# Kernel tuning notes

Hardware: AMD Instinct MI355X
Metric: run time of the kernel (lower is better)

The kernel has to match this reference:

```python
import jax, jax.numpy as jnp
import numpy as np

NUM_USERS = 100000
NUM_ITEMS = 50000
NUM_LAYERS = 4
DIM_H = 64
E_HALF = 2000000  # undirected interactions; symmetrized to 4M directed edges


def setup_inputs() -> dict:
    key = jax.random.key(0)
    k1, k2, k3, k4 = jax.random.split(key, 4)
    emb_users = 0.01 * jax.random.normal(k1, (NUM_USERS, DIM_H), dtype=jnp.float32)
    emb_items = 0.01 * jax.random.normal(k2, (NUM_ITEMS, DIM_H), dtype=jnp.float32)
    u = jax.random.randint(k3, (E_HALF,), 0, NUM_USERS, dtype=jnp.int64)
    it = jax.random.randint(k4, (E_HALF,), 0, NUM_ITEMS, dtype=jnp.int64) + NUM_USERS
    # bidirectional bipartite graph, as LightGCN expects
    src = jnp.concatenate([u, it])
    dst = jnp.concatenate([it, u])
    edge_index = jnp.stack([src, dst])  # [2, 4M]
    return {"emb_users": emb_users, "emb_items": emb_items, "edge_index": edge_index}


def reference(emb_users, emb_items, edge_index):
    N = emb_users.shape[0] + emb_items.shape[0]
    src, dst = edge_index[0], edge_index[1]
    # gcn_norm (add_self_loops=False): w_e = deg[src]^-1/2 * deg[dst]^-1/2
    deg = jax.ops.segment_sum(jnp.ones(src.shape[0], dtype=emb_users.dtype), dst, num_segments=N)
    dis = jnp.where(deg > 0, deg ** -0.5, 0.0).astype(emb_users.dtype)
    w = (dis[src] * dis[dst])[:, None]  # [E,1]

    emb = jnp.concatenate([emb_users, emb_items])  # [N, D]
    embs_sum = emb
    x = emb
    for _ in range(NUM_LAYERS):
        x = jax.ops.segment_sum(w * x[src], dst, num_segments=N)  # LGConv
        embs_sum = embs_sum + x
    # original: 1/(L+1) * mean over L+1 stacked layers -> sum / (L+1)^2
    emb_final = embs_sum / float((NUM_LAYERS + 1) ** 2)
    emb_users_final = emb_final[: emb_users.shape[0]]
    emb_items_final = emb_final[emb_users.shape[0]:]
    return (emb_users_final, emb_users, emb_items_final, emb_items)
```

## Files before the change

### kernel.cpp

```cpp
#include <hip/hip_runtime.h>
#include <hip/hip_fp8.h>
#include <hip/hip_fp16.h>

typedef unsigned char u8;
typedef unsigned short u16;
typedef float v2f __attribute__((ext_vector_type(2)));

#define SCAN_B 256

#define NPB      128
#define NPB_SH   7
#define P2_CAP   6144
#define STG_CAP  6144
#define P1_CHUNK 16384
#define P1_T     256
#define P1_IT    (P1_CHUNK / P1_T)
#define NB_MAX   2048
#define STG_OFF  ((size_t)20 << 20)

static __device__ __forceinline__ float fp8_to_f32(u8 b) {
    __hip_fp8_e4m3 t;
    t.__x = (__hip_fp8_storage_t)b;
    return (float)t;
}
static __device__ __forceinline__ u8 f32_to_fp8(float v) {
    __hip_fp8_e4m3 t(v);
    return (u8)t.__x;
}
static __device__ __forceinline__ float h2f(u16 u) {
    __half_raw r; r.x = u;
    return __half2float(__half(r));
}
static __device__ __forceinline__ u16 f2h(float f) {
    __half h = __float2half_rn(f);
    __half_raw r = (__half_raw)h;
    return r.x;
}

template <bool HI>
static __device__ __forceinline__ v2f pk2(unsigned w) {
#if __has_builtin(__builtin_amdgcn_cvt_pk_f32_fp8)
    return __builtin_amdgcn_cvt_pk_f32_fp8((int)w, HI);
#else
    v2f r;
    r.x = fp8_to_f32(HI ? (u8)(w >> 16) : (u8)(w));
    r.y = fp8_to_f32(HI ? (u8)(w >> 24) : (u8)(w >> 8));
    return r;
#endif
}

__global__ void detect_kernel(const int* __restrict__ edges, int* __restrict__ flag) {
    __shared__ int cnt[256];
    int t = threadIdx.x;
    int c = 0;
    for (int i = t; i < 32768; i += 256)
        if (edges[2 * i + 1] != 0) c++;
    cnt[t] = c;
    __syncthreads();
    for (int off = 128; off > 0; off >>= 1) {
        if (t < off) cnt[t] += cnt[t + off];
        __syncthreads();
    }
    if (t == 0) flag[0] = (cnt[0] < 8) ? 2 : 1;
}

__global__ void gcur_fixed_init(int* __restrict__ gcur, int NB) {
    int b = blockIdx.x * blockDim.x + threadIdx.x;
    if (b < NB) gcur[b] = b * STG_CAP;
}

__global__ void part1_kernel(const int* __restrict__ edges, const int* __restrict__ flag,
                             int* __restrict__ gcur, unsigned* __restrict__ staging,
                             int E, int NB) {
    __shared__ int lcount[NB_MAX];
    __shared__ int lbase[NB_MAX];
    int t = threadIdx.x;
    int s = flag[0];
    long e0 = (long)blockIdx.x * P1_CHUNK;
    const int* dptr = edges + (long)E * s;
    for (int b = t; b < NB; b += P1_T) lcount[b] = 0;
    __syncthreads();
    for (int j = 0; j < P1_IT; j += 8) {
        int dv[8]; bool vl[8];
        #pragma unroll
        for (int k = 0; k < 8; ++k) {
            long e = e0 + (long)(j + k) * P1_T + t;
            vl[k] = (e < E);
            dv[k] = vl[k] ? dptr[e * s] : 0;
        }
        #pragma unroll
        for (int k = 0; k < 8; ++k)
            if (vl[k]) atomicAdd(&lcount[dv[k] >> NPB_SH], 1);
    }
    __syncthreads();
    for (int b = t; b < NB; b += P1_T) {
        int c = lcount[b];
        lbase[b] = (c > 0) ? atomicAdd(&gcur[b], c) : 0;
        lcount[b] = 0;
    }
    __syncthreads();
    for (int j = 0; j < P1_IT; j += 8) {
        int dv[8], sv[8]; bool vl[8];
        #pragma unroll
        for (int k = 0; k < 8; ++k) {
            long e = e0 + (long)(j + k) * P1_T + t;
            vl[k] = (e < E);
            dv[k] = vl[k] ? dptr[e * s] : 0;
            sv[k] = vl[k] ? edges[e * s] : 0;
        }
        #pragma unroll
        for (int k = 0; k < 8; ++k) {
            if (vl[k]) {
                int b = dv[k] >> NPB_SH;
                int slot = atomicAdd(&lcount[b], 1);
                int pos = lbase[b] + slot;
                if (pos < (b + 1) * STG_CAP)
                    staging[pos] = (unsigned)sv[k]
                                 | ((unsigned)(dv[k] & (NPB - 1)) << 20);
            }
        }
    }
}

__global__ void bucket_scan_kernel(const int* __restrict__ gcur, int* __restrict__ bbase,
                                   int NB) {
    __shared__ int sh[2][1024];
    int t = threadIdx.x;
    int i0 = 2 * t, i1 = 2 * t + 1;
    int a0 = (i0 < NB) ? (gcur[i0] - i0 * STG_CAP) : 0;
    int a1 = (i1 < NB) ? (gcur[i1] - i1 * STG_CAP) : 0;
    sh[0][t] = a0 + a1;
    __syncthreads();
    int src = 0;
    for (int off = 1; off < 1024; off <<= 1) {
        int x = sh[src][t] + ((t >= off) ? sh[src][t - off] : 0);
        sh[src ^ 1][t] = x;
        src ^= 1;
        __syncthreads();
    }
    int incl = sh[src][t];
    int excl = incl - (a0 + a1);
    if (i0 < NB) bbase[i0] = excl;
    if (i1 < NB) bbase[i1] = excl + a0;
    if (t == 1023) bbase[NB] = incl;
}

__global__ void __launch_bounds__(256) part2a_kernel(
        const int* __restrict__ gcur, const int* __restrict__ bbase,
        const unsigned* __restrict__ staging, int* __restrict__ row_ptr,
        float* __restrict__ dis, int n, int E, int NB) {
    __shared__ int cnt[NPB];
    __shared__ int sc[2][NPB];
    int b = blockIdx.x;
    int t = threadIdx.x;
    int dlo = b << NPB_SH;
    int sbase = b * STG_CAP;
    int c = gcur[b] - sbase;
    int base = bbase[b];
    if (t < NPB) cnt[t] = 0;
    __syncthreads();
    for (int k = t; k < c; k += 256) {
        unsigned wd = staging[sbase + k];
        atomicAdd(&cnt[wd >> 20], 1);
    }
    __syncthreads();
    if (t < NPB) sc[0][t] = cnt[t];
    __syncthreads();
    int src = 0;
    for (int off = 1; off < NPB; off <<= 1) {
        if (t < NPB) {
            int x = sc[src][t] + ((t >= off) ? sc[src][t - off] : 0);
            sc[src ^ 1][t] = x;
        }
        src ^= 1;
        __syncthreads();
    }
    if (t < NPB) {
        int node = dlo + t;
        if (node < n) {
            int d = cnt[t];
            row_ptr[node] = base + sc[src][t] - d;
            dis[node] = (d > 0) ? rsqrtf((float)d) : 0.0f;
        }
    }
    if (b == 0 && t == 0) row_ptr[n] = E;
}

__global__ void __launch_bounds__(256) part2b_kernel(
        const int* __restrict__ row_ptr, const int* __restrict__ gcur,
        const unsigned* __restrict__ staging, const float* __restrict__ dis,
        int2* __restrict__ cw, int n) {
    __shared__ int2 win[P2_CAP];
    __shared__ int cur[NPB];
    int b = blockIdx.x;
    int t = threadIdx.x;
    int dlo = b << NPB_SH;
    int sbase = b * STG_CAP;
    int cnt = gcur[b] - sbase;
    int base = row_ptr[dlo];
    if (t < NPB) {
        int node = dlo + t;
        cur[t] = (node < n) ? (row_ptr[node] - base) : 0;
    }
    __syncthreads();
    if (cnt <= P2_CAP) {
        for (int k = t; k < cnt; k += 256) {
            unsigned wd = staging[sbase + k];
            int sv = wd & 0xFFFFF;
            int dloc = wd >> 20;
            float w = dis[sv] * dis[dlo + dloc];
            int p = atomicAdd(&cur[dloc], 1);
            win[p] = make_int2(sv, __float_as_int(w));
        }
        __syncthreads();
        for (int k = t; k < cnt; k += 256)
            cw[base + k] = win[k];
    } else {
        for (int k = t; k < cnt; k += 256) {
            unsigned wd = staging[sbase + k];
            int sv = wd & 0xFFFFF;
            int dloc = wd >> 20;
            float w = dis[sv] * dis[dlo + dloc];
            int p = atomicAdd(&cur[dloc], 1);
            cw[base + p] = make_int2(sv, __float_as_int(w));
        }
    }
}

__global__ void count_deg_kernel(const int* __restrict__ edges, const int* __restrict__ flag,
                                 int* __restrict__ deg, int E) {
    int e = blockIdx.x * blockDim.x + threadIdx.x;
    if (e >= E) return;
    int s = flag[0];
    int d = edges[(long)E * s + (long)e * s];
    atomicAdd(&deg[d], 1);
}

__global__ void scan_phase1(const int* __restrict__ deg, int* __restrict__ row_ptr,
                            int* __restrict__ bsum, int n) {
    __shared__ int sh[2][SCAN_B];
    int t = threadIdx.x;
    int gi = blockIdx.x * SCAN_B + t;
    int v = (gi < n) ? deg[gi] : 0;
    int src = 0;
    sh[0][t] = v;
    __syncthreads();
    for (int off = 1; off < SCAN_B; off <<= 1) {
        int x = sh[src][t] + ((t >= off) ? sh[src][t - off] : 0);
        sh[src ^ 1][t] = x;
        src ^= 1;
        __syncthreads();
    }
    int incl = sh[src][t];
    if (gi < n) row_ptr[gi] = incl - v;
    if (t == SCAN_B - 1) bsum[blockIdx.x] = incl;
}

__global__ void scan_phase2(int* __restrict__ bsum, int nb) {
    __shared__ int sh[1024];
    int t = threadIdx.x;
    sh[t] = (t < nb) ? bsum[t] : 0;
    __syncthreads();
    if (t == 0) {
        int acc = 0;
        for (int i = 0; i < nb; ++i) { int x = sh[i]; sh[i] = acc; acc += x; }
    }
    __syncthreads();
    if (t < nb) bsum[t] = sh[t];
}

__global__ void scan_phase3(const int* __restrict__ deg, const int* __restrict__ bsum,
                            int* __restrict__ row_ptr, int* __restrict__ cursor,
                            float* __restrict__ dis, int n, int E) {
    int gi = blockIdx.x * SCAN_B + threadIdx.x;
    if (gi < n) {
        int e = row_ptr[gi] + bsum[blockIdx.x];
        row_ptr[gi] = e;
        cursor[gi]  = e;
        int d = deg[gi];
        dis[gi] = (d > 0) ? rsqrtf((float)d) : 0.0f;
    }
    if (gi == 0) row_ptr[n] = E;
}

__global__ void scatter_kernel(const int* __restrict__ edges, const int* __restrict__ flag,
                               const float* __restrict__ dis, int* __restrict__ cursor,
                               int2* __restrict__ cw, int E) {
    int e = blockIdx.x * blockDim.x + threadIdx.x;
    if (e >= E) return;
    int s = flag[0];
    int sv = edges[(long)e * s];
    int dv = edges[(long)E * s + (long)e * s];
    float w = dis[sv] * dis[dv];
    int pos = atomicAdd(&cursor[dv], 1);
    cw[pos] = make_int2(sv, __float_as_int(w));
}

__global__ void init_kernel(const float* __restrict__ eu, const float* __restrict__ ei,
                            u8* __restrict__ x0, long NU64, long tot) {
    long i = (long)blockIdx.x * blockDim.x + threadIdx.x;
    if (i >= tot) return;
    float v = (i < NU64) ? eu[i] : ei[i - NU64];
    x0[i] = f32_to_fp8(v);
}

__global__ void spmm_kernel(const int* __restrict__ row_ptr, const int2* __restrict__ cw,
                            const u8* __restrict__ xin, u8* __restrict__ xout, int n) {
    int wave = (blockIdx.x * blockDim.x + threadIdx.x) >> 6;
    int lane = threadIdx.x & 63;
    if (wave >= n) return;
    int beg = row_ptr[wave], end = row_ptr[wave + 1];
    int g = lane >> 3;
    int h = lane & 7;

    float a0 = 0.f, a1 = 0.f, a2 = 0.f, a3 = 0.f;
    float a4 = 0.f, a5 = 0.f, a6 = 0.f, a7 = 0.f;

    for (int iA = beg + g; iA < end; iA += 16) {
        int iB = iA + 8;
        bool vB = iB < end;
        int2 ca = cw[iA];
        int2 cb = cw[vB ? iB : iA];
        uint2 dA = *(const uint2*)(xin + ((long)ca.x << 6) + (h << 3));
        uint2 dB = *(const uint2*)(xin + ((long)cb.x << 6) + (h << 3));
        float wA = __int_as_float(ca.y);
        float wB = vB ? __int_as_float(cb.y) : 0.0f;
        v2f pA0 = pk2<false>(dA.x), pA1 = pk2<true>(dA.x);
        v2f pA2 = pk2<false>(dA.y), pA3 = pk2<true>(dA.y);
        v2f pB0 = pk2<false>(dB.x), pB1 = pk2<true>(dB.x);
        v2f pB2 = pk2<false>(dB.y), pB3 = pk2<true>(dB.y);
        a0 = fmaf(wA, pA0.x, a0); a1 = fmaf(wA, pA0.y, a1);
        a2 = fmaf(wA, pA1.x, a2); a3 = fmaf(wA, pA1.y, a3);
        a4 = fmaf(wA, pA2.x, a4); a5 = fmaf(wA, pA2.y, a5);
        a6 = fmaf(wA, pA3.x, a6); a7 = fmaf(wA, pA3.y, a7);
        a0 = fmaf(wB, pB0.x, a0); a1 = fmaf(wB, pB0.y, a1);
        a2 = fmaf(wB, pB1.x, a2); a3 = fmaf(wB, pB1.y, a3);
        a4 = fmaf(wB, pB2.x, a4); a5 = fmaf(wB, pB2.y, a5);
        a6 = fmaf(wB, pB3.x, a6); a7 = fmaf(wB, pB3.y, a7);
    }
    a0 += __shfl_xor(a0, 8);  a1 += __shfl_xor(a1, 8);
    a2 += __shfl_xor(a2, 8);  a3 += __shfl_xor(a3, 8);
    a4 += __shfl_xor(a4, 8);  a5 += __shfl_xor(a5, 8);
    a6 += __shfl_xor(a6, 8);  a7 += __shfl_xor(a7, 8);
    a0 += __shfl_xor(a0, 16); a1 += __shfl_xor(a1, 16);
    a2 += __shfl_xor(a2, 16); a3 += __shfl_xor(a3, 16);
    a4 += __shfl_xor(a4, 16); a5 += __shfl_xor(a5, 16);
    a6 += __shfl_xor(a6, 16); a7 += __shfl_xor(a7, 16);
    a0 += __shfl_xor(a0, 32); a1 += __shfl_xor(a1, 32);
    a2 += __shfl_xor(a2, 32); a3 += __shfl_xor(a3, 32);
    a4 += __shfl_xor(a4, 32); a5 += __shfl_xor(a5, 32);
    a6 += __shfl_xor(a6, 32); a7 += __shfl_xor(a7, 32);
    if (g == 0) {
        unsigned lo = (unsigned)f32_to_fp8(a0) | ((unsigned)f32_to_fp8(a1) << 8)
                    | ((unsigned)f32_to_fp8(a2) << 16) | ((unsigned)f32_to_fp8(a3) << 24);
        unsigned hi = (unsigned)f32_to_fp8(a4) | ((unsigned)f32_to_fp8(a5) << 8)
                    | ((unsigned)f32_to_fp8(a6) << 16) | ((unsigned)f32_to_fp8(a7) << 24);
        *(uint2*)(xout + ((long)wave << 6) + (h << 3)) = make_uint2(lo, hi);
    }
}

__global__ void final_kernel(const u8* __restrict__ x1, const u8* __restrict__ x2,
                             const u8* __restrict__ x3, const u8* __restrict__ x4,
                             const float* __restrict__ eu, const float* __restrict__ ei,
                             float* __restrict__ out, long NU64, long NI64) {
    long i = (long)blockIdx.x * blockDim.x + threadIdx.x;
    if (i >= NU64 + NI64) return;
    float base = (i < NU64) ? eu[i] : ei[i - NU64];
    float s = base + fp8_to_f32(x1[i]) + fp8_to_f32(x2[i])
                   + fp8_to_f32(x3[i]) + fp8_to_f32(x4[i]);
    float v = s * (1.0f / 25.0f);
    if (i < NU64) {
        out[i] = v;
        out[NU64 + i] = base;
    } else {
        long j = i - NU64;
        out[2 * NU64 + j] = v;
        out[2 * NU64 + NI64 + j] = base;
    }
}

__global__ void init16_kernel(const float* __restrict__ eu, const float* __restrict__ ei,
                              u16* __restrict__ x0, long NU64, long tot) {
    long i = (long)blockIdx.x * blockDim.x + threadIdx.x;
    if (i >= tot) return;
    float v = (i < NU64) ? eu[i] : ei[i - NU64];
    x0[i] = f2h(v);
}

__global__ void spmm16_kernel(const int* __restrict__ row_ptr, const int2* __restrict__ cw,
                              const u16* __restrict__ xin, u16* __restrict__ xout, int n) {
    int wave = (blockIdx.x * blockDim.x + threadIdx.x) >> 6;
    int lane = threadIdx.x & 63;
    if (wave >= n) return;
    int beg = row_ptr[wave], end = row_ptr[wave + 1];
    int g = lane >> 3;
    int h = lane & 7;

    float a0 = 0.f, a1 = 0.f, a2 = 0.f, a3 = 0.f;
    float a4 = 0.f, a5 = 0.f, a6 = 0.f, a7 = 0.f;
    const char* xb = (const char*)xin;

    for (int iA = beg + g; iA < end; iA += 16) {
        int iB = iA + 8;
        bool vB = iB < end;
        int2 ca = cw[iA];
        int2 cb = cw[vB ? iB : iA];
        uint4 dA = *(const uint4*)(xb + ((long)ca.x << 7) + (h << 4));
        uint4 dB = *(const uint4*)(xb + ((long)cb.x << 7) + (h << 4));
        float wA = __int_as_float(ca.y);
        float wB = vB ? __int_as_float(cb.y) : 0.0f;
        a0 = fmaf(wA, h2f((u16)dA.x), a0);  a1 = fmaf(wA, h2f((u16)(dA.x >> 16)), a1);
        a2 = fmaf(wA, h2f((u16)dA.y), a2);  a3 = fmaf(wA, h2f((u16)(dA.y >> 16)), a3);
        a4 = fmaf(wA, h2f((u16)dA.z), a4);  a5 = fmaf(wA, h2f((u16)(dA.z >> 16)), a5);
        a6 = fmaf(wA, h2f((u16)dA.w), a6);  a7 = fmaf(wA, h2f((u16)(dA.w >> 16)), a7);
        a0 = fmaf(wB, h2f((u16)dB.x), a0);  a1 = fmaf(wB, h2f((u16)(dB.x >> 16)), a1);
        a2 = fmaf(wB, h2f((u16)dB.y), a2);  a3 = fmaf(wB, h2f((u16)(dB.y >> 16)), a3);
        a4 = fmaf(wB, h2f((u16)dB.z), a4);  a5 = fmaf(wB, h2f((u16)(dB.z >> 16)), a5);
        a6 = fmaf(wB, h2f((u16)dB.w), a6);  a7 = fmaf(wB, h2f((u16)(dB.w >> 16)), a7);
    }

    a0 += __shfl_xor(a0, 8);  a1 += __shfl_xor(a1, 8);
    a2 += __shfl_xor(a2, 8);  a3 += __shfl_xor(a3, 8);
    a4 += __shfl_xor(a4, 8);  a5 += __shfl_xor(a5, 8);
    a6 += __shfl_xor(a6, 8);  a7 += __shfl_xor(a7, 8);
    a0 += __shfl_xor(a0, 16); a1 += __shfl_xor(a1, 16);
    a2 += __shfl_xor(a2, 16); a3 += __shfl_xor(a3, 16);
    a4 += __shfl_xor(a4, 16); a5 += __shfl_xor(a5, 16);
    a6 += __shfl_xor(a6, 16); a7 += __shfl_xor(a7, 16);
    a0 += __shfl_xor(a0, 32); a1 += __shfl_xor(a1, 32);
    a2 += __shfl_xor(a2, 32); a3 += __shfl_xor(a3, 32);
    a4 += __shfl_xor(a4, 32); a5 += __shfl_xor(a5, 32);
    a6 += __shfl_xor(a6, 32); a7 += __shfl_xor(a7, 32);

    if (g == 0) {
        uint4 ov;
        ov.x = (unsigned)f2h(a0) | ((unsigned)f2h(a1) << 16);
        ov.y = (unsigned)f2h(a2) | ((unsigned)f2h(a3) << 16);
        ov.z = (unsigned)f2h(a4) | ((unsigned)f2h(a5) << 16);
        ov.w = (unsigned)f2h(a6) | ((unsigned)f2h(a7) << 16);
        *(uint4*)((char*)xout + ((long)wave << 7) + (h << 4)) = ov;
    }
}

__global__ void final16_kernel(const u16* __restrict__ x1, const u16* __restrict__ x2,
                               const u16* __restrict__ x3, const u16* __restrict__ x4,
                               const float* __restrict__ eu, const float* __restrict__ ei,
                               float* __restrict__ out, long NU64, long NI64) {
    long i = (long)blockIdx.x * blockDim.x + threadIdx.x;
    if (i >= NU64 + NI64) return;
    float base = (i < NU64) ? eu[i] : ei[i - NU64];
    float s = base + h2f(x1[i]) + h2f(x2[i]) + h2f(x3[i]) + h2f(x4[i]);
    float v = s * (1.0f / 25.0f);
    if (i < NU64) {
        out[i] = v;
        out[NU64 + i] = base;
    } else {
        long j = i - NU64;
        out[2 * NU64 + j] = v;
        out[2 * NU64 + NI64 + j] = base;
    }
}

extern "C" void kernel_launch(void* const* d_in, const int* in_sizes, int n_in,
                              void* d_out, int out_size, void* d_ws, size_t ws_size,
                              hipStream_t stream) {
    const float* eu = (const float*)d_in[0];
    const float* ei = (const float*)d_in[1];
    const int* edges = (const int*)d_in[2];
    float* out = (float*)d_out;

    const int NU = in_sizes[0] / 64;
    const int NI = in_sizes[1] / 64;
    const int N  = NU + NI;
    const int E  = in_sizes[2] / 2;
    const int NB = (N + NPB - 1) / NPB;

    char* w = (char*)d_ws;
    size_t off = 0;
    auto alloc = [&](size_t bytes) -> void* {
        void* p = w + off;
        off += (bytes + 255) & ~(size_t)255;
        return p;
    };
    int*   flag    = (int*)  alloc(256);
    int*   deg     = (int*)  alloc((size_t)N * 4);
    int*   row_ptr = (int*)  alloc((size_t)(N + 1) * 4);
    int*   cursor  = (int*)  alloc((size_t)N * 4);
    float* dis     = (float*)alloc((size_t)N * 4);
    int*   bsum    = (int*)  alloc(1024 * 4);
    int*   gcur    = (int*)  alloc((size_t)(NB + 1) * 4);
    int*   bbase   = (int*)  alloc((size_t)(NB + 1) * 4);
    int2*  cw      = (int2*) alloc((size_t)E * 8);
    const long NU64 = (long)NU * 64, NI64 = (long)NI * 64;
    const long tot = NU64 + NI64;

    const size_t xb16 = ((size_t)tot * 2 + 255) & ~(size_t)255;
    const size_t xb8  = ((size_t)tot + 255) & ~(size_t)255;
    const bool use16 = (off + 4 * xb16) <= ws_size;
    const size_t xb = use16 ? xb16 : xb8;
    char* x1 = (char*)alloc(xb);
    char* x2 = (char*)alloc(xb);
    char* x3 = (char*)alloc(xb);
    char* x4 = (char*)alloc(xb);

    const size_t out_bytes = (size_t)tot * 8;
    char*     x0      = (char*)out;
    unsigned* staging = (unsigned*)((char*)out + STG_OFF);

    detect_kernel<<<1, 256, 0, stream>>>(edges, flag);

    const size_t x0_bytes = use16 ? (size_t)tot * 2 : (size_t)tot;
    bool fast = (NB <= NB_MAX) && (N < (1 << 20)) &&
                (STG_OFF + (size_t)NB * STG_CAP * 4 <= out_bytes) &&
                (x0_bytes <= STG_OFF);

    if (fast) {
        gcur_fixed_init<<<(NB + 255) / 256, 256, 0, stream>>>(gcur, NB);
        part1_kernel<<<(E + P1_CHUNK - 1) / P1_CHUNK, P1_T, 0, stream>>>(edges, flag, gcur,
                                                                         staging, E, NB);
        bucket_scan_kernel<<<1, 1024, 0, stream>>>(gcur, bbase, NB);
        part2a_kernel<<<NB, 256, 0, stream>>>(gcur, bbase, staging, row_ptr, dis, N, E, NB);
        part2b_kernel<<<NB, 256, 0, stream>>>(row_ptr, gcur, staging, dis, cw, N);
    } else {
        const int nb = (N + SCAN_B - 1) / SCAN_B;
        hipMemsetAsync(deg, 0, (size_t)N * 4, stream);
        count_deg_kernel<<<(E + 255) / 256, 256, 0, stream>>>(edges, flag, deg, E);
        scan_phase1<<<nb, SCAN_B, 0, stream>>>(deg, row_ptr, bsum, N);
        scan_phase2<<<1, 1024, 0, stream>>>(bsum, nb);
        scan_phase3<<<nb, SCAN_B, 0, stream>>>(deg, bsum, row_ptr, cursor, dis, N, E);
        scatter_kernel<<<(E + 255) / 256, 256, 0, stream>>>(edges, flag, dis, cursor, cw, E);
    }

    const int nblk = (N + 3) / 4;
    const int eblk = (int)((tot + 255) / 256);
    if (use16) {
        init16_kernel<<<eblk, 256, 0, stream>>>(eu, ei, (u16*)x0, NU64, tot);
        spmm16_kernel<<<nblk, 256, 0, stream>>>(row_ptr, cw, (u16*)x0, (u16*)x1, N);
        spmm16_kernel<<<nblk, 256, 0, stream>>>(row_ptr, cw, (u16*)x1, (u16*)x2, N);
        spmm16_kernel<<<nblk, 256, 0, stream>>>(row_ptr, cw, (u16*)x2, (u16*)x3, N);
        spmm16_kernel<<<nblk, 256, 0, stream>>>(row_ptr, cw, (u16*)x3, (u16*)x4, N);
        final16_kernel<<<eblk, 256, 0, stream>>>((u16*)x1, (u16*)x2, (u16*)x3, (u16*)x4,
                                                 eu, ei, out, NU64, NI64);
    } else {
        init_kernel<<<eblk, 256, 0, stream>>>(eu, ei, (u8*)x0, NU64, tot);
        spmm_kernel<<<nblk, 256, 0, stream>>>(row_ptr, cw, (u8*)x0, (u8*)x1, N);
        spmm_kernel<<<nblk, 256, 0, stream>>>(row_ptr, cw, (u8*)x1, (u8*)x2, N);
        spmm_kernel<<<nblk, 256, 0, stream>>>(row_ptr, cw, (u8*)x2, (u8*)x3, N);
        spmm_kernel<<<nblk, 256, 0, stream>>>(row_ptr, cw, (u8*)x3, (u8*)x4, N);
        final_kernel<<<eblk, 256, 0, stream>>>((u8*)x1, (u8*)x2, (u8*)x3, (u8*)x4,
                                               eu, ei, out, NU64, NI64);
    }
}
```

Before: 562.6 us.

## Factor edge weights into per-node scaling and store column indices only

Rewrites propagation in a pre-scaled basis, u = D^-1/2 x. Each SpMM then sums plain neighbor rows and scales by 1/deg at the end, and the final kernel rescales by sqrt(deg). This drops the per-edge weight from the CSR, halving edge-array traffic (int instead of int2) and removing the weight computation and gathers in part2b. It also spaces out the global bucket counters to reduce atomic contention, and the scaling adds an extra rounding step to the half/fp8 intermediates.

New measurement: 583.4 us. 3.7% more time.

```diff
diff --git a/kernel.cpp b/kernel.cpp
--- a/kernel.cpp
+++ b/kernel.cpp
@@ -4,7 +4,6 @@
 
 typedef unsigned char u8;
 typedef unsigned short u16;
-typedef float v2f __attribute__((ext_vector_type(2)));
 
 #define SCAN_B 256
 
@@ -16,7 +15,9 @@
 #define P1_T     256
 #define P1_IT    (P1_CHUNK / P1_T)
 #define NB_MAX   2048
+#define GC_STR   16
 #define STG_OFF  ((size_t)20 << 20)
+#define FP8_SCALE 16.0f
 
 static __device__ __forceinline__ float fp8_to_f32(u8 b) {
     __hip_fp8_e4m3 t;
@@ -37,18 +38,6 @@
     return r.x;
 }
 
-template <bool HI>
-static __device__ __forceinline__ v2f pk2(unsigned w) {
-#if __has_builtin(__builtin_amdgcn_cvt_pk_f32_fp8)
-    return __builtin_amdgcn_cvt_pk_f32_fp8((int)w, HI);
-#else
-    v2f r;
-    r.x = fp8_to_f32(HI ? (u8)(w >> 16) : (u8)(w));
-    r.y = fp8_to_f32(HI ? (u8)(w >> 24) : (u8)(w >> 8));
-    return r;
-#endif
-}
-
 __global__ void detect_kernel(const int* __restrict__ edges, int* __restrict__ flag) {
     __shared__ int cnt[256];
     int t = threadIdx.x;
@@ -66,7 +55,7 @@
 
 __global__ void gcur_fixed_init(int* __restrict__ gcur, int NB) {
     int b = blockIdx.x * blockDim.x + threadIdx.x;
-    if (b < NB) gcur[b] = b * STG_CAP;
+    if (b < NB) gcur[b * GC_STR] = b * STG_CAP;
 }
 
 __global__ void part1_kernel(const int* __restrict__ edges, const int* __restrict__ flag,
@@ -95,7 +84,7 @@
     __syncthreads();
     for (int b = t; b < NB; b += P1_T) {
         int c = lcount[b];
-        lbase[b] = (c > 0) ? atomicAdd(&gcur[b], c) : 0;
+        lbase[b] = (c > 0) ? atomicAdd(&gcur[b * GC_STR], c) : 0;
         lcount[b] = 0;
     }
     __syncthreads();
@@ -127,8 +116,8 @@
     __shared__ int sh[2][1024];
     int t = threadIdx.x;
     int i0 = 2 * t, i1 = 2 * t + 1;
-    int a0 = (i0 < NB) ? (gcur[i0] - i0 * STG_CAP) : 0;
-    int a1 = (i1 < NB) ? (gcur[i1] - i1 * STG_CAP) : 0;
+    int a0 = (i0 < NB) ? (gcur[i0 * GC_STR] - i0 * STG_CAP) : 0;
+    int a1 = (i1 < NB) ? (gcur[i1 * GC_STR] - i1 * STG_CAP) : 0;
     sh[0][t] = a0 + a1;
     __syncthreads();
     int src = 0;
@@ -148,14 +137,15 @@
 __global__ void __launch_bounds__(256) part2a_kernel(
         const int* __restrict__ gcur, const int* __restrict__ bbase,
         const unsigned* __restrict__ staging, int* __restrict__ row_ptr,
-        float* __restrict__ dis, int n, int E, int NB) {
+        float* __restrict__ dis, float* __restrict__ dis2, float* __restrict__ invd,
+        int n, int E, int NB) {
     __shared__ int cnt[NPB];
     __shared__ int sc[2][NPB];
     int b = blockIdx.x;
     int t = threadIdx.x;
     int dlo = b << NPB_SH;
     int sbase = b * STG_CAP;
-    int c = gcur[b] - sbase;
+    int c = gcur[b * GC_STR] - sbase;
     int base = bbase[b];
     if (t < NPB) cnt[t] = 0;
     __syncthreads();
@@ -180,7 +170,10 @@
         if (node < n) {
             int d = cnt[t];
             row_ptr[node] = base + sc[src][t] - d;
-            dis[node] = (d > 0) ? rsqrtf((float)d) : 0.0f;
+            float ds = (d > 0) ? rsqrtf((float)d) : 0.0f;
+            dis[node]  = ds;
+            dis2[node] = ds * ds;
+            invd[node] = (d > 0) ? sqrtf((float)d) : 0.0f;
         }
     }
     if (b == 0 && t == 0) row_ptr[n] = E;
@@ -188,15 +181,14 @@
 
 __global__ void __launch_bounds__(256) part2b_kernel(
         const int* __restrict__ row_ptr, const int* __restrict__ gcur,
-        const unsigned* __restrict__ staging, const float* __restrict__ dis,
-        int2* __restrict__ cw, int n) {
-    __shared__ int2 win[P2_CAP];
+        const unsigned* __restrict__ staging, int* __restrict__ cs, int n) {
+    __shared__ int win[P2_CAP];
     __shared__ int cur[NPB];
     int b = blockIdx.x;
     int t = threadIdx.x;
     int dlo = b << NPB_SH;
     int sbase = b * STG_CAP;
-    int cnt = gcur[b] - sbase;
+    int cnt = gcur[b * GC_STR] - sbase;
     int base = row_ptr[dlo];
     if (t < NPB) {
         int node = dlo + t;
@@ -206,23 +198,17 @@
     if (cnt <= P2_CAP) {
         for (int k = t; k < cnt; k += 256) {
             unsigned wd = staging[sbase + k];
-            int sv = wd & 0xFFFFF;
-            int dloc = wd >> 20;
-            float w = dis[sv] * dis[dlo + dloc];
-            int p = atomicAdd(&cur[dloc], 1);
-            win[p] = make_int2(sv, __float_as_int(w));
+            int p = atomicAdd(&cur[wd >> 20], 1);
+            win[p] = (int)(wd & 0xFFFFF);
         }
         __syncthreads();
         for (int k = t; k < cnt; k += 256)
-            cw[base + k] = win[k];
+            cs[base + k] = win[k];
     } else {
         for (int k = t; k < cnt; k += 256) {
             unsigned wd = staging[sbase + k];
-            int sv = wd & 0xFFFFF;
-            int dloc = wd >> 20;
-            float w = dis[sv] * dis[dlo + dloc];
-            int p = atomicAdd(&cur[dloc], 1);
-            cw[base + p] = make_int2(sv, __float_as_int(w));
+            int p = atomicAdd(&cur[wd >> 20], 1);
+            cs[base + p] = (int)(wd & 0xFFFFF);
         }
     }
 }
@@ -271,41 +257,45 @@
 
 __global__ void scan_phase3(const int* __restrict__ deg, const int* __restrict__ bsum,
                             int* __restrict__ row_ptr, int* __restrict__ cursor,
-                            float* __restrict__ dis, int n, int E) {
+                            float* __restrict__ dis, float* __restrict__ dis2,
+                            float* __restrict__ invd, int n, int E) {
     int gi = blockIdx.x * SCAN_B + threadIdx.x;
     if (gi < n) {
         int e = row_ptr[gi] + bsum[blockIdx.x];
         row_ptr[gi] = e;
         cursor[gi]  = e;
         int d = deg[gi];
-        dis[gi] = (d > 0) ? rsqrtf((float)d) : 0.0f;
+        float ds = (d > 0) ? rsqrtf((float)d) : 0.0f;
+        dis[gi]  = ds;
+        dis2[gi] = ds * ds;
+        invd[gi] = (d > 0) ? sqrtf((float)d) : 0.0f;
     }
     if (gi == 0) row_ptr[n] = E;
 }
 
 __global__ void scatter_kernel(const int* __restrict__ edges, const int* __restrict__ flag,
-                               const float* __restrict__ dis, int* __restrict__ cursor,
-                               int2* __restrict__ cw, int E) {
+                               int* __restrict__ cursor, int* __restrict__ cs, int E) {
     int e = blockIdx.x * blockDim.x + threadIdx.x;
     if (e >= E) return;
     int s = flag[0];
     int sv = edges[(long)e * s];
     int dv = edges[(long)E * s + (long)e * s];
-    float w = dis[sv] * dis[dv];
     int pos = atomicAdd(&cursor[dv], 1);
-    cw[pos] = make_int2(sv, __float_as_int(w));
-}
-
-__global__ void init_kernel(const float* __restrict__ eu, const float* __restrict__ ei,
-                            u8* __restrict__ x0, long NU64, long tot) {
+    cs[pos] = sv;
+}
+
+__global__ void init16_kernel(const float* __restrict__ eu, const float* __restrict__ ei,
+                              const float* __restrict__ dis,
+                              u16* __restrict__ u0, long NU64, long tot) {
     long i = (long)blockIdx.x * blockDim.x + threadIdx.x;
     if (i >= tot) return;
     float v = (i < NU64) ? eu[i] : ei[i - NU64];
-    x0[i] = f32_to_fp8(v);
-}
-
-__global__ void spmm_kernel(const int* __restrict__ row_ptr, const int2* __restrict__ cw,
-                            const u8* __restrict__ xin, u8* __restrict__ xout, int n) {
+    u0[i] = f2h(v * dis[i >> 6]);
+}
+
+__global__ void spmm16_kernel(const int* __restrict__ row_ptr, const int* __restrict__ cs,
+                              const u16* __restrict__ uin, u16* __restrict__ uout,
+                              const float* __restrict__ dis2, int n) {
     int wave = (blockIdx.x * blockDim.x + threadIdx.x) >> 6;
     int lane = threadIdx.x & 63;
     if (wave >= n) return;
@@ -315,28 +305,111 @@
 
     float a0 = 0.f, a1 = 0.f, a2 = 0.f, a3 = 0.f;
     float a4 = 0.f, a5 = 0.f, a6 = 0.f, a7 = 0.f;
+    const char* xb = (const char*)uin;
 
     for (int iA = beg + g; iA < end; iA += 16) {
         int iB = iA + 8;
         bool vB = iB < end;
-        int2 ca = cw[iA];
-        int2 cb = cw[vB ? iB : iA];
-        uint2 dA = *(const uint2*)(xin + ((long)ca.x << 6) + (h << 3));
-        uint2 dB = *(const uint2*)(xin + ((long)cb.x << 6) + (h << 3));
-        float wA = __int_as_float(ca.y);
-        float wB = vB ? __int_as_float(cb.y) : 0.0f;
-        v2f pA0 = pk2<false>(dA.x), pA1 = pk2<true>(dA.x);
-        v2f pA2 = pk2<false>(dA.y), pA3 = pk2<true>(dA.y);
-        v2f pB0 = pk2<false>(dB.x), pB1 = pk2<true>(dB.x);
-        v2f pB2 = pk2<false>(dB.y), pB3 = pk2<true>(dB.y);
-        a0 = fmaf(wA, pA0.x, a0); a1 = fmaf(wA, pA0.y, a1);
-        a2 = fmaf(wA, pA1.x, a2); a3 = fmaf(wA, pA1.y, a3);
-        a4 = fmaf(wA, pA2.x, a4); a5 = fmaf(wA, pA2.y, a5);
-        a6 = fmaf(wA, pA3.x, a6); a7 = fmaf(wA, pA3.y, a7);
-        a0 = fmaf(wB, pB0.x, a0); a1 = fmaf(wB, pB0.y, a1);
-        a2 = fmaf(wB, pB1.x, a2); a3 = fmaf(wB, pB1.y, a3);
-        a4 = fmaf(wB, pB2.x, a4); a5 = fmaf(wB, pB2.y, a5);
-        a6 = fmaf(wB, pB3.x, a6); a7 = fmaf(wB, pB3.y, a7);
+        int sa = cs[iA];
+        int sb = cs[vB ? iB : iA];
+        uint4 dA = *(const uint4*)(xb + ((long)sa << 7) + (h << 4));
+        uint4 dB = *(const uint4*)(xb + ((long)sb << 7) + (h << 4));
+        float mB = vB ? 1.0f : 0.0f;
+        a0 += h2f((u16)dA.x);  a1 += h2f((u16)(dA.x >> 16));
+        a2 += h2f((u16)dA.y);  a3 += h2f((u16)(dA.y >> 16));
+        a4 += h2f((u16)dA.z);  a5 += h2f((u16)(dA.z >> 16));
+        a6 += h2f((u16)dA.w);  a7 += h2f((u16)(dA.w >> 16));
+        a0 = fmaf(mB, h2f((u16)dB.x), a0);  a1 = fmaf(mB, h2f((u16)(dB.x >> 16)), a1);
+        a2 = fmaf(mB, h2f((u16)dB.y), a2);  a3 = fmaf(mB, h2f((u16)(dB.y >> 16)), a3);
+        a4 = fmaf(mB, h2f((u16)dB.z), a4);  a5 = fmaf(mB, h2f((u16)(dB.z >> 16)), a5);
+        a6 = fmaf(mB, h2f((u16)dB.w), a6);  a7 = fmaf(mB, h2f((u16)(dB.w >> 16)), a7);
+    }
+
+    a0 += __shfl_xor(a0, 8);  a1 += __shfl_xor(a1, 8);
+    a2 += __shfl_xor(a2, 8);  a3 += __shfl_xor(a3, 8);
+    a4 += __shfl_xor(a4, 8);  a5 += __shfl_xor(a5, 8);
+    a6 += __shfl_xor(a6, 8);  a7 += __shfl_xor(a7, 8);
+    a0 += __shfl_xor(a0, 16); a1 += __shfl_xor(a1, 16);
+    a2 += __shfl_xor(a2, 16); a3 += __shfl_xor(a3, 16);
+    a4 += __shfl_xor(a4, 16); a5 += __shfl_xor(a5, 16);
+    a6 += __shfl_xor(a6, 16); a7 += __shfl_xor(a7, 16);
+    a0 += __shfl_xor(a0, 32); a1 += __shfl_xor(a1, 32);
+    a2 += __shfl_xor(a2, 32); a3 += __shfl_xor(a3, 32);
+    a4 += __shfl_xor(a4, 32); a5 += __shfl_xor(a5, 32);
+    a6 += __shfl_xor(a6, 32); a7 += __shfl_xor(a7, 32);
+
+    if (g == 0) {
+        float s2 = dis2[wave];
+        uint4 ov;
+        ov.x = (unsigned)f2h(a0 * s2) | ((unsigned)f2h(a1 * s2) << 16);
+        ov.y = (unsigned)f2h(a2 * s2) | ((unsigned)f2h(a3 * s2) << 16);
+        ov.z = (unsigned)f2h(a4 * s2) | ((unsigned)f2h(a5 * s2) << 16);
+        ov.w = (unsigned)f2h(a6 * s2) | ((unsigned)f2h(a7 * s2) << 16);
+        *(uint4*)((char*)uout + ((long)wave << 7) + (h << 4)) = ov;
+    }
+}
+
+__global__ void final16_kernel(const u16* __restrict__ u1, const u16* __restrict__ u2,
+                               const u16* __restrict__ u3, const u16* __restrict__ u4,
+                               const float* __restrict__ eu, const float* __restrict__ ei,
+                               const float* __restrict__ invd,
+                               float* __restrict__ out, long NU64, long NI64) {
+    long i = (long)blockIdx.x * blockDim.x + threadIdx.x;
+    if (i >= NU64 + NI64) return;
+    float base = (i < NU64) ? eu[i] : ei[i - NU64];
+    float us = h2f(u1[i]) + h2f(u2[i]) + h2f(u3[i]) + h2f(u4[i]);
+    float s = base + us * invd[i >> 6];
+    float v = s * (1.0f / 25.0f);
+    if (i < NU64) {
+        out[i] = v;
+        out[NU64 + i] = base;
+    } else {
+        long j = i - NU64;
+        out[2 * NU64 + j] = v;
+        out[2 * NU64 + NI64 + j] = base;
+    }
+}
+
+__global__ void init8_kernel(const float* __restrict__ eu, const float* __restrict__ ei,
+                             const float* __restrict__ dis,
+                             u8* __restrict__ u0, long NU64, long tot) {
+    long i = (long)blockIdx.x * blockDim.x + threadIdx.x;
+    if (i >= tot) return;
+    float v = (i < NU64) ? eu[i] : ei[i - NU64];
+    u0[i] = f32_to_fp8(v * dis[i >> 6] * FP8_SCALE);
+}
+
+__global__ void spmm8_kernel(const int* __restrict__ row_ptr, const int* __restrict__ cs,
+                             const u8* __restrict__ uin, u8* __restrict__ uout,
+                             const float* __restrict__ dis2, int n) {
+    int wave = (blockIdx.x * blockDim.x + threadIdx.x) >> 6;
+    int lane = threadIdx.x & 63;
+    if (wave >= n) return;
+    int beg = row_ptr[wave], end = row_ptr[wave + 1];
+    int g = lane >> 3;
+    int h = lane & 7;
+    float a0 = 0.f, a1 = 0.f, a2 = 0.f, a3 = 0.f;
+    float a4 = 0.f, a5 = 0.f, a6 = 0.f, a7 = 0.f;
+    for (int iA = beg + g; iA < end; iA += 16) {
+        int iB = iA + 8;
+        bool vB = iB < end;
+        int sa = cs[iA];
+        int sb = cs[vB ? iB : iA];
+        uint2 dA = *(const uint2*)(uin + ((long)sa << 6) + (h << 3));
+        uint2 dB = *(const uint2*)(uin + ((long)sb << 6) + (h << 3));
+        float mB = vB ? 1.0f : 0.0f;
+        a0 += fp8_to_f32((u8)dA.x);         a1 += fp8_to_f32((u8)(dA.x >> 8));
+        a2 += fp8_to_f32((u8)(dA.x >> 16)); a3 += fp8_to_f32((u8)(dA.x >> 24));
+        a4 += fp8_to_f32((u8)dA.y);         a5 += fp8_to_f32((u8)(dA.y >> 8));
+        a6 += fp8_to_f32((u8)(dA.y >> 16)); a7 += fp8_to_f32((u8)(dA.y >> 24));
+        a0 = fmaf(mB, fp8_to_f32((u8)dB.x), a0);
+        a1 = fmaf(mB, fp8_to_f32((u8)(dB.x >> 8)), a1);
+        a2 = fmaf(mB, fp8_to_f32((u8)(dB.x >> 16)), a2);
+        a3 = fmaf(mB, fp8_to_f32((u8)(dB.x >> 24)), a3);
+        a4 = fmaf(mB, fp8_to_f32((u8)dB.y), a4);
+        a5 = fmaf(mB, fp8_to_f32((u8)(dB.y >> 8)), a5);
+        a6 = fmaf(mB, fp8_to_f32((u8)(dB.y >> 16)), a6);
+        a7 = fmaf(mB, fp8_to_f32((u8)(dB.y >> 24)), a7);
     }
     a0 += __shfl_xor(a0, 8);  a1 += __shfl_xor(a1, 8);
     a2 += __shfl_xor(a2, 8);  a3 += __shfl_xor(a3, 8);
@@ -351,105 +424,25 @@
     a4 += __shfl_xor(a4, 32); a5 += __shfl_xor(a5, 32);
     a6 += __shfl_xor(a6, 32); a7 += __shfl_xor(a7, 32);
     if (g == 0) {
-        unsigned lo = (unsigned)f32_to_fp8(a0) | ((unsigned)f32_to_fp8(a1) << 8)
-                    | ((unsigned)f32_to_fp8(a2) << 16) | ((unsigned)f32_to_fp8(a3) << 24);
-        unsigned hi = (unsigned)f32_to_fp8(a4) | ((unsigned)f32_to_fp8(a5) << 8)
-                    | ((unsigned)f32_to_fp8(a6) << 16) | ((unsigned)f32_to_fp8(a7) << 24);
-        *(uint2*)(xout + ((long)wave << 6) + (h << 3)) = make_uint2(lo, hi);
-    }
-}
-
-__global__ void final_kernel(const u8* __restrict__ x1, const u8* __restrict__ x2,
-                             const u8* __restrict__ x3, const u8* __restrict__ x4,
-                             const float* __restrict__ eu, const float* __restrict__ ei,
-                             float* __restrict__ out, long NU64, long NI64) {
+        float s2 = dis2[wave];
+        unsigned lo = (unsigned)f32_to_fp8(a0 * s2) | ((unsigned)f32_to_fp8(a1 * s2) << 8)
+                    | ((unsigned)f32_to_fp8(a2 * s2) << 16) | ((unsigned)f32_to_fp8(a3 * s2) << 24);
+        unsigned hi = (unsigned)f32_to_fp8(a4 * s2) | ((unsigned)f32_to_fp8(a5 * s2) << 8)
+                    | ((unsigned)f32_to_fp8(a6 * s2) << 16) | ((unsigned)f32_to_fp8(a7 * s2) << 24);
+        *(uint2*)(uout + ((long)wave << 6) + (h << 3)) = make_uint2(lo, hi);
+    }
+}
+
+__global__ void final8_kernel(const u8* __restrict__ u1, const u8* __restrict__ u2,
+                              const u8* __restrict__ u3, const u8* __restrict__ u4,
+                              const float* __restrict__ eu, const float* __restrict__ ei,
+                              const float* __restrict__ invd,
+                              float* __restrict__ out, long NU64, long NI64) {
     long i = (long)blockIdx.x * blockDim.x + threadIdx.x;
     if (i >= NU64 + NI64) return;
     float base = (i < NU64) ? eu[i] : ei[i - NU64];
-    float s = base + fp8_to_f32(x1[i]) + fp8_to_f32(x2[i])
-                   + fp8_to_f32(x3[i]) + fp8_to_f32(x4[i]);
-    float v = s * (1.0f / 25.0f);
-    if (i < NU64) {
-        out[i] = v;
-        out[NU64 + i] = base;
-    } else {
-        long j = i - NU64;
-        out[2 * NU64 + j] = v;
-        out[2 * NU64 + NI64 + j] = base;
-    }
-}
-
-__global__ void init16_kernel(const float* __restrict__ eu, const float* __restrict__ ei,
-                              u16* __restrict__ x0, long NU64, long tot) {
-    long i = (long)blockIdx.x * blockDim.x + threadIdx.x;
-    if (i >= tot) return;
-    float v = (i < NU64) ? eu[i] : ei[i - NU64];
-    x0[i] = f2h(v);
-}
-
-__global__ void spmm16_kernel(const int* __restrict__ row_ptr, const int2* __restrict__ cw,
-                              const u16* __restrict__ xin, u16* __restrict__ xout, int n) {
-    int wave = (blockIdx.x * blockDim.x + threadIdx.x) >> 6;
-    int lane = threadIdx.x & 63;
-    if (wave >= n) return;
-    int beg = row_ptr[wave], end = row_ptr[wave + 1];
-    int g = lane >> 3;
-    int h = lane & 7;
-
-    float a0 = 0.f, a1 = 0.f, a2 = 0.f, a3 = 0.f;
-    float a4 = 0.f, a5 = 0.f, a6 = 0.f, a7 = 0.f;
-    const char* xb = (const char*)xin;
-
-    for (int iA = beg + g; iA < end; iA += 16) {
-        int iB = iA + 8;
-        bool vB = iB < end;
-        int2 ca = cw[iA];
-        int2 cb = cw[vB ? iB : iA];
-        uint4 dA = *(const uint4*)(xb + ((long)ca.x << 7) + (h << 4));
-        uint4 dB = *(const uint4*)(xb + ((long)cb.x << 7) + (h << 4));
-        float wA = __int_as_float(ca.y);
-        float wB = vB ? __int_as_float(cb.y) : 0.0f;
-        a0 = fmaf(wA, h2f((u16)dA.x), a0);  a1 = fmaf(wA, h2f((u16)(dA.x >> 16)), a1);
-        a2 = fmaf(wA, h2f((u16)dA.y), a2);  a3 = fmaf(wA, h2f((u16)(dA.y >> 16)), a3);
-        a4 = fmaf(wA, h2f((u16)dA.z), a4);  a5 = fmaf(wA, h2f((u16)(dA.z >> 16)), a5);
-        a6 = fmaf(wA, h2f((u16)dA.w), a6);  a7 = fmaf(wA, h2f((u16)(dA.w >> 16)), a7);
-        a0 = fmaf(wB, h2f((u16)dB.x), a0);  a1 = fmaf(wB, h2f((u16)(dB.x >> 16)), a1);
-        a2 = fmaf(wB, h2f((u16)dB.y), a2);  a3 = fmaf(wB, h2f((u16)(dB.y >> 16)), a3);
-        a4 = fmaf(wB, h2f((u16)dB.z), a4);  a5 = fmaf(wB, h2f((u16)(dB.z >> 16)), a5);
-        a6 = fmaf(wB, h2f((u16)dB.w), a6);  a7 = fmaf(wB, h2f((u16)(dB.w >> 16)), a7);
-    }
-
-    a0 += __shfl_xor(a0, 8);  a1 += __shfl_xor(a1, 8);
-    a2 += __shfl_xor(a2, 8);  a3 += __shfl_xor(a3, 8);
-    a4 += __shfl_xor(a4, 8);  a5 += __shfl_xor(a5, 8);
-    a6 += __shfl_xor(a6, 8);  a7 += __shfl_xor(a7, 8);
-    a0 += __shfl_xor(a0, 16); a1 += __shfl_xor(a1, 16);
-    a2 += __shfl_xor(a2, 16); a3 += __shfl_xor(a3, 16);
-    a4 += __shfl_xor(a4, 16); a5 += __shfl_xor(a5, 16);
-    a6 += __shfl_xor(a6, 16); a7 += __shfl_xor(a7, 16);
-    a0 += __shfl_xor(a0, 32); a1 += __shfl_xor(a1, 32);
-    a2 += __shfl_xor(a2, 32); a3 += __shfl_xor(a3, 32);
-    a4 += __shfl_xor(a4, 32); a5 += __shfl_xor(a5, 32);
-    a6 += __shfl_xor(a6, 32); a7 += __shfl_xor(a7, 32);
-
-    if (g == 0) {
-        uint4 ov;
-        ov.x = (unsigned)f2h(a0) | ((unsigned)f2h(a1) << 16);
-        ov.y = (unsigned)f2h(a2) | ((unsigned)f2h(a3) << 16);
-        ov.z = (unsigned)f2h(a4) | ((unsigned)f2h(a5) << 16);
-        ov.w = (unsigned)f2h(a6) | ((unsigned)f2h(a7) << 16);
-        *(uint4*)((char*)xout + ((long)wave << 7) + (h << 4)) = ov;
-    }
-}
-
-__global__ void final16_kernel(const u16* __restrict__ x1, const u16* __restrict__ x2,
-                               const u16* __restrict__ x3, const u16* __restrict__ x4,
-                               const float* __restrict__ eu, const float* __restrict__ ei,
-                               float* __restrict__ out, long NU64, long NI64) {
-    long i = (long)blockIdx.x * blockDim.x + threadIdx.x;
-    if (i >= NU64 + NI64) return;
-    float base = (i < NU64) ? eu[i] : ei[i - NU64];
-    float s = base + h2f(x1[i]) + h2f(x2[i]) + h2f(x3[i]) + h2f(x4[i]);
+    float us = fp8_to_f32(u1[i]) + fp8_to_f32(u2[i]) + fp8_to_f32(u3[i]) + fp8_to_f32(u4[i]);
+    float s = base + us * invd[i >> 6] * (1.0f / FP8_SCALE);
     float v = s * (1.0f / 25.0f);
     if (i < NU64) {
         out[i] = v;
@@ -487,10 +480,12 @@
     int*   row_ptr = (int*)  alloc((size_t)(N + 1) * 4);
     int*   cursor  = (int*)  alloc((size_t)N * 4);
     float* dis     = (float*)alloc((size_t)N * 4);
+    float* dis2    = (float*)alloc((size_t)N * 4);
+    float* invd    = (float*)alloc((size_t)N * 4);
     int*   bsum    = (int*)  alloc(1024 * 4);
-    int*   gcur    = (int*)  alloc((size_t)(NB + 1) * 4);
+    int*   gcur    = (int*)  alloc((size_t)(NB + 1) * GC_STR * 4);
     int*   bbase   = (int*)  alloc((size_t)(NB + 1) * 4);
-    int2*  cw      = (int2*) alloc((size_t)E * 8);
+    int*   cs      = (int*)  alloc((size_t)E * 4);
     const long NU64 = (long)NU * 64, NI64 = (long)NI * 64;
     const long tot = NU64 + NI64;
 
@@ -519,35 +514,37 @@
         part1_kernel<<<(E + P1_CHUNK - 1) / P1_CHUNK, P1_T, 0, stream>>>(edges, flag, gcur,
                                                                          staging, E, NB);
         bucket_scan_kernel<<<1, 1024, 0, stream>>>(gcur, bbase, NB);
-        part2a_kernel<<<NB, 256, 0, stream>>>(gcur, bbase, staging, row_ptr, dis, N, E, NB);
-        part2b_kernel<<<NB, 256, 0, stream>>>(row_ptr, gcur, staging, dis, cw, N);
+        part2a_kernel<<<NB, 256, 0, stream>>>(gcur, bbase, staging, row_ptr,
+                                              dis, dis2, invd, N, E, NB);
+        part2b_kernel<<<NB, 256, 0, stream>>>(row_ptr, gcur, staging, cs, N);
     } else {
         const int nb = (N + SCAN_B - 1) / SCAN_B;
         hipMemsetAsync(deg, 0, (size_t)N * 4, stream);
         count_deg_kernel<<<(E + 255) / 256, 256, 0, stream>>>(edges, flag, deg, E);
         scan_phase1<<<nb, SCAN_B, 0, stream>>>(deg, row_ptr, bsum, N);
         scan_phase2<<<1, 1024, 0, stream>>>(bsum, nb);
-        scan_phase3<<<nb, SCAN_B, 0, stream>>>(deg, bsum, row_ptr, cursor, dis, N, E);
-        scatter_kernel<<<(E + 255) / 256, 256, 0, stream>>>(edges, flag, dis, cursor, cw, E);
+        scan_phase3<<<nb, SCAN_B, 0, stream>>>(deg, bsum, row_ptr, cursor,
+                                               dis, dis2, invd, N, E);
+        scatter_kernel<<<(E + 255) / 256, 256, 0, stream>>>(edges, flag, cursor, cs, E);
     }
 
     const int nblk = (N + 3) / 4;
     const int eblk = (int)((tot + 255) / 256);
     if (use16) {
-        init16_kernel<<<eblk, 256, 0, stream>>>(eu, ei, (u16*)x0, NU64, tot);
-        spmm16_kernel<<<nblk, 256, 0, stream>>>(row_ptr, cw, (u16*)x0, (u16*)x1, N);
-        spmm16_kernel<<<nblk, 256, 0, stream>>>(row_ptr, cw, (u16*)x1, (u16*)x2, N);
-        spmm16_kernel<<<nblk, 256, 0, stream>>>(row_ptr, cw, (u16*)x2, (u16*)x3, N);
-        spmm16_kernel<<<nblk, 256, 0, stream>>>(row_ptr, cw, (u16*)x3, (u16*)x4, N);
+        init16_kernel<<<eblk, 256, 0, stream>>>(eu, ei, dis, (u16*)x0, NU64, tot);
+        spmm16_kernel<<<nblk, 256, 0, stream>>>(row_ptr, cs, (u16*)x0, (u16*)x1, dis2, N);
+        spmm16_kernel<<<nblk, 256, 0, stream>>>(row_ptr, cs, (u16*)x1, (u16*)x2, dis2, N);
+        spmm16_kernel<<<nblk, 256, 0, stream>>>(row_ptr, cs, (u16*)x2, (u16*)x3, dis2, N);
+        spmm16_kernel<<<nblk, 256, 0, stream>>>(row_ptr, cs, (u16*)x3, (u16*)x4, dis2, N);
         final16_kernel<<<eblk, 256, 0, stream>>>((u16*)x1, (u16*)x2, (u16*)x3, (u16*)x4,
-                                                 eu, ei, out, NU64, NI64);
+                                                 eu, ei, invd, out, NU64, NI64);
     } else {
-        init_kernel<<<eblk, 256, 0, stream>>>(eu, ei, (u8*)x0, NU64, tot);
-        spmm_kernel<<<nblk, 256, 0, stream>>>(row_ptr, cw, (u8*)x0, (u8*)x1, N);
-        spmm_kernel<<<nblk, 256, 0, stream>>>(row_ptr, cw, (u8*)x1, (u8*)x2, N);
-        spmm_kernel<<<nblk, 256, 0, stream>>>(row_ptr, cw, (u8*)x2, (u8*)x3, N);
-        spmm_kernel<<<nblk, 256, 0, stream>>>(row_ptr, cw, (u8*)x3, (u8*)x4, N);
-        final_kernel<<<eblk, 256, 0, stream>>>((u8*)x1, (u8*)x2, (u8*)x3, (u8*)x4,
-                                               eu, ei, out, NU64, NI64);
-    }
-}
+        init8_kernel<<<eblk, 256, 0, stream>>>(eu, ei, dis, (u8*)x0, NU64, tot);
+        spmm8_kernel<<<nblk, 256, 0, stream>>>(row_ptr, cs, (u8*)x0, (u8*)x1, dis2, N);
+        spmm8_kernel<<<nblk, 256, 0, stream>>>(row_ptr, cs, (u8*)x1, (u8*)x2, dis2, N);
+        spmm8_kernel<<<nblk, 256, 0, stream>>>(row_ptr, cs, (u8*)x2, (u8*)x3, dis2, N);
+        spmm8_kernel<<<nblk, 256, 0, stream>>>(row_ptr, cs, (u8*)x3, (u8*)x4, dis2, N);
+        final8_kernel<<<eblk, 256, 0, stream>>>((u8*)x1, (u8*)x2, (u8*)x3, (u8*)x4,
+                                                eu, ei, invd, out, NU64, NI64);
+    }
+}
```
